# Optimization experiments

Measured on AMD Instinct MI355X. Metric: run time of the kernel, lower is better.

Reference implementation:

```python
import jax, jax.numpy as jnp
import numpy as np

GROUP_SIZE = 128


def setup_inputs() -> dict:
    key = jax.random.key(0)
    k0, k1, k2, k3 = jax.random.split(key, 4)
    B, S, I, O, G = 4, 2048, 4096, 11008, GROUP_SIZE
    x = jax.random.normal(k0, (B, S, I), dtype=jnp.float32)
    # int4 values in [-8, 7]
    qweight = jax.random.randint(k1, (O, I), -8, 8, dtype=jnp.int32)
    # group-wise positive scales, shape [O, I // G]
    scales = jax.random.uniform(k2, (O, I // G), dtype=jnp.float32,
                                minval=1e-3, maxval=2e-2)
    bias = jax.random.normal(k3, (O,), dtype=jnp.float32) * 0.01
    return {"x": x, "qweight": qweight, "scales": scales, "bias": bias}


def reference(x, qweight, scales, bias):
    # bits == 4, quantized path: group-wise dequant then linear
    O, I = qweight.shape
    G = GROUP_SIZE
    w = qweight.reshape(O, I // G, G).astype(x.dtype) * scales[:, :, None].astype(x.dtype)
    w = w.reshape(O, I)  # dequantized weight [O, I]
    # F.linear: y = x @ w.T + bias
    return jnp.einsum('bsi,oi->bso', x, w) + bias.astype(x.dtype)
```

## Files before the change

### kernel.cpp

```cpp
#include <hip/hip_runtime.h>
#include <hip/hip_bf16.h>


typedef __bf16 bf16_t;
typedef __bf16 bf16x8 __attribute__((ext_vector_type(8)));
typedef float f32x4 __attribute__((ext_vector_type(4)));
typedef int ix4 __attribute__((ext_vector_type(4)));
typedef __attribute__((address_space(3))) unsigned char lds_byte;
typedef __attribute__((address_space(1))) unsigned char gmem_byte;

__global__ void rowquant_kernel(const float* __restrict__ x, int* __restrict__ xq,
                                float* __restrict__ sx, int I) {
  __shared__ float red[256];
  const int m = blockIdx.x;
  const float* row = x + (size_t)m * I;
  float mx = 0.f;
  for (int c = threadIdx.x * 4; c < I; c += 1024) {
    const float4 f = *reinterpret_cast<const float4*>(row + c);
    mx = fmaxf(mx, fmaxf(fmaxf(fabsf(f.x), fabsf(f.y)), fmaxf(fabsf(f.z), fabsf(f.w))));
  }
  red[threadIdx.x] = mx;
  __syncthreads();
#pragma unroll
  for (int s = 128; s > 0; s >>= 1) {
    if (threadIdx.x < s) red[threadIdx.x] = fmaxf(red[threadIdx.x], red[threadIdx.x + s]);
    __syncthreads();
  }
  const float rm = fmaxf(red[0], 1e-30f);
  if (threadIdx.x == 0) sx[m] = rm * (1.f / 127.f);
  const float inv = 127.f / rm;
  int* orow = xq + (size_t)m * (I >> 2);
  for (int c = threadIdx.x * 4; c < I; c += 1024) {
    const float4 f = *reinterpret_cast<const float4*>(row + c);
    const int b0 = (int)rintf(f.x * inv), b1 = (int)rintf(f.y * inv);
    const int b2 = (int)rintf(f.z * inv), b3 = (int)rintf(f.w * inv);
    orow[c >> 2] = (b0 & 255) | ((b1 & 255) << 8) | ((b2 & 255) << 16) | (b3 << 24);
  }
}

__global__ void colscale_kernel(const float* __restrict__ sc, float* __restrict__ tw,
                                int NG, int O) {
  const int n = blockIdx.x * blockDim.x + threadIdx.x;
  if (n >= O) return;
  const float* row = sc + (size_t)n * NG;
  float mx = 0.f;
  for (int g = 0; g < NG; ++g) mx = fmaxf(mx, row[g]);
  tw[n] = fmaxf(mx, 1e-30f) * (8.f / 127.f);
}

__global__ void quant_w_kernel(const int* __restrict__ qw, const float* __restrict__ sc,
                               const float* __restrict__ tw, int* __restrict__ wq,
                               int I, int G, long n16) {
  const long stride = (long)gridDim.x * blockDim.x;
  const int I16 = I / 16;
  for (long i = (long)blockIdx.x * blockDim.x + threadIdx.x; i < n16; i += stride) {
    const int n = (int)(i / I16);
    const int k0 = (int)((i - (long)n * I16) * 16);
    const float f = sc[(size_t)n * (I / G) + k0 / G] / tw[n];
    const int4* p = reinterpret_cast<const int4*>(qw + (size_t)n * I + k0);
    const int4 q0 = p[0], q1 = p[1], q2 = p[2], q3 = p[3];
    int b[16];
    b[0] = (int)rintf((float)q0.x * f); b[1] = (int)rintf((float)q0.y * f);
    b[2] = (int)rintf((float)q0.z * f); b[3] = (int)rintf((float)q0.w * f);
    b[4] = (int)rintf((float)q1.x * f); b[5] = (int)rintf((float)q1.y * f);
    b[6] = (int)rintf((float)q1.z * f); b[7] = (int)rintf((float)q1.w * f);
    b[8] = (int)rintf((float)q2.x * f); b[9] = (int)rintf((float)q2.y * f);
    b[10] = (int)rintf((float)q2.z * f); b[11] = (int)rintf((float)q2.w * f);
    b[12] = (int)rintf((float)q3.x * f); b[13] = (int)rintf((float)q3.y * f);
    b[14] = (int)rintf((float)q3.z * f); b[15] = (int)rintf((float)q3.w * f);
    int4 o;
    o.x = (b[0] & 255) | ((b[1] & 255) << 8) | ((b[2] & 255) << 16) | (b[3] << 24);
    o.y = (b[4] & 255) | ((b[5] & 255) << 8) | ((b[6] & 255) << 16) | (b[7] << 24);
    o.z = (b[8] & 255) | ((b[9] & 255) << 8) | ((b[10] & 255) << 16) | (b[11] << 24);
    o.w = (b[12] & 255) | ((b[13] & 255) << 8) | ((b[14] & 255) << 16) | (b[15] << 24);
    reinterpret_cast<int4*>(wq)[i] = o;
  }
}


#define WAITV(n) asm volatile("s_waitcnt vmcnt(" #n ")" ::: "memory")
#define WAITL(n) asm volatile("s_waitcnt lgkmcnt(" #n ")" ::: "memory")
#define BAR() __builtin_amdgcn_s_barrier()
#define SETP(n) __builtin_amdgcn_s_setprio(n)

#define RD_A(DB, q) do { \
  _Pragma("unroll") \
  for (int i_ = 0; i_ < 4; ++i_) { \
    aF[i_][0] = *reinterpret_cast<const ix4*>(&ldsb[(DB) + aRd + (unsigned)((q) * 64 + i_ * 16) * 128u + ks0]); \
    aF[i_][1] = *reinterpret_cast<const ix4*>(&ldsb[(DB) + aRd + (unsigned)((q) * 64 + i_ * 16) * 128u + ks1]); \
  } \
} while (0)

#define RD_B(DB, nh, BF) do { \
  _Pragma("unroll") \
  for (int j_ = 0; j_ < 2; ++j_) { \
    BF[j_][0] = *reinterpret_cast<const ix4*>(&ldsb[(DB) + bRd + (unsigned)((nh) * 32 + j_ * 16) * 128u + ks0]); \
    BF[j_][1] = *reinterpret_cast<const ix4*>(&ldsb[(DB) + bRd + (unsigned)((nh) * 32 + j_ * 16) * 128u + ks1]); \
  } \
} while (0)

#define STG(BASE, P, tau) do { \
  __builtin_amdgcn_global_load_lds((const gmem_byte*)((P) + (size_t)(tau) * 128), \
                                   (lds_byte*)&ldsb[(BASE) + wOff], 16, 0, 0); \
  __builtin_amdgcn_global_load_lds((const gmem_byte*)((P) + (size_t)64 * K + (size_t)(tau) * 128), \
                                   (lds_byte*)&ldsb[(BASE) + 8192u + wOff], 16, 0, 0); \
} while (0)

#define MMQI(q, nh, BF) do { \
  _Pragma("unroll") \
  for (int i_ = 0; i_ < 4; ++i_) \
  _Pragma("unroll") \
  for (int j_ = 0; j_ < 2; ++j_) { \
    acc[(q) * 4 + i_][(nh) * 2 + j_] = __builtin_amdgcn_mfma_i32_16x16x64_i8(aF[i_][0], BF[j_][0], acc[(q) * 4 + i_][(nh) * 2 + j_], 0, 0, 0); \
    acc[(q) * 4 + i_][(nh) * 2 + j_] = __builtin_amdgcn_mfma_i32_16x16x64_i8(aF[i_][1], BF[j_][1], acc[(q) * 4 + i_][(nh) * 2 + j_], 0, 0, 0); \
  } \
} while (0)

__launch_bounds__(512, 2)
__global__ void gemm256_i8_kernel(const char* __restrict__ A, const char* __restrict__ B,
                                  const float* __restrict__ sx, const float* __restrict__ tw,
                                  const float* __restrict__ bias, float* __restrict__ C,
                                  int M, int N, int K) {
  __shared__ __align__(16) unsigned char ldsb[131072];

  const int tid = threadIdx.x;
  const int lane = tid & 63;
  const int w = tid >> 6;
  const int wr = w >> 2;
  const int wc = w & 3;

  const int MT = M >> 8;
  int mt, nt;
  const int bid = blockIdx.x;
  if ((MT & 7) == 0) {
    const int xcd = bid & 7, idx = bid >> 3;
    const int mpx = MT >> 3;
    nt = idx / mpx;
    mt = xcd * mpx + (idx - nt * mpx);
  } else {
    mt = bid % MT;
    nt = bid / MT;
  }
  const int m0 = mt << 8, n0 = nt << 8;

  const int srow8 = lane >> 3;
  const int scol16 = (lane & 7) ^ (srow8 & 7);
  const char* aP0 = A + (size_t)(m0 + w * 8 + srow8) * K + scol16 * 16;
  const char* aP1 = aP0 + (size_t)128 * K;
  const char* bP0 = B + (size_t)(n0 + w * 8 + srow8) * K + scol16 * 16;
  const char* bP1 = bP0 + (size_t)128 * K;
  const unsigned wOff = (unsigned)w * 1024u;

  const unsigned fr = lane & 15;
  const unsigned hi16 = (unsigned)lane >> 4;
  const unsigned sw_ = (fr & 7u) << 4;
  const unsigned ks0 = (hi16 * 16u) ^ sw_;
  const unsigned ks1 = (64u + hi16 * 16u) ^ sw_;
  const unsigned aRd = (unsigned)wr * 16384u + fr * 128u;
  const unsigned bRd = 32768u + (unsigned)(wc >> 1) * 16384u +
                       ((unsigned)(wc & 1) * 64u + fr) * 128u;

  ix4 acc[8][4];
#pragma unroll
  for (int i = 0; i < 8; ++i)
#pragma unroll
    for (int j = 0; j < 4; ++j) acc[i][j] = (ix4){0, 0, 0, 0};

  ix4 aF[4][2], bF0[2][2], bF1[2][2];

  const int NITER = K >> 8;

  STG(0u, aP0, 0); STG(16384u, aP1, 0); STG(32768u, bP0, 0); STG(49152u, bP1, 0);
  STG(98304u, bP0, 1); STG(114688u, bP1, 1);
  WAITV(4);
  BAR();

  for (int it = 0; it < NITER - 1; ++it) {
    const int t = 2 * it;
    RD_A(0u, 0); RD_B(0u, 0, bF0); RD_B(0u, 1, bF1);
    STG(65536u, aP0, t + 1); STG(81920u, aP1, t + 1);
    BAR(); WAITL(0);
    SETP(1); MMQI(0, 0, bF0); MMQI(0, 1, bF1); SETP(0); BAR();
    RD_A(0u, 1);
    STG(32768u, bP0, t + 2); STG(49152u, bP1, t + 2);
    WAITV(4);
    BAR(); WAITL(0);
    SETP(1); MMQI(1, 0, bF0); MMQI(1, 1, bF1); SETP(0); BAR();
    RD_A(65536u, 0); RD_B(65536u, 0, bF0); RD_B(65536u, 1, bF1);
    STG(0u, aP0, t + 2); STG(16384u, aP1, t + 2);
    BAR(); WAITL(0);
    SETP(1); MMQI(0, 0, bF0); MMQI(0, 1, bF1); SETP(0); BAR();
    RD_A(65536u, 1);
    STG(98304u, bP0, t + 3); STG(114688u, bP1, t + 3);
    WAITV(4);
    BAR(); WAITL(0);
    SETP(1); MMQI(1, 0, bF0); MMQI(1, 1, bF1); SETP(0); BAR();
  }
  {
    RD_A(0u, 0); RD_B(0u, 0, bF0); RD_B(0u, 1, bF1);
    STG(65536u, aP0, 2 * NITER - 1); STG(81920u, aP1, 2 * NITER - 1);
    BAR(); WAITL(0);
    SETP(1); MMQI(0, 0, bF0); MMQI(0, 1, bF1); SETP(0); BAR();
    RD_A(0u, 1);
    WAITV(0);
    BAR(); WAITL(0);
    SETP(1); MMQI(1, 0, bF0); MMQI(1, 1, bF1); SETP(0); BAR();
    RD_A(65536u, 0); RD_B(65536u, 0, bF0); RD_B(65536u, 1, bF1);
    WAITL(0);
    SETP(1); MMQI(0, 0, bF0); MMQI(0, 1, bF1); SETP(0);
    RD_A(65536u, 1);
    WAITL(0);
    SETP(1); MMQI(1, 0, bF0); MMQI(1, 1, bF1); SETP(0);
  }

  const int row0 = m0 + wr * 128 + ((lane >> 4) << 2);
  const int col0 = n0 + wc * 64 + (lane & 15);
  float sxc[8][4];
#pragma unroll
  for (int hi = 0; hi < 8; ++hi) {
    const int rbase = row0 + (hi >> 2) * 64 + (hi & 3) * 16;
#pragma unroll
    for (int r = 0; r < 4; ++r) sxc[hi][r] = sx[rbase + r];
  }
#pragma unroll
  for (int j = 0; j < 4; ++j) {
    const int n = col0 + j * 16;
    const float tn = tw[n];
    const float bv = bias[n];
#pragma unroll
    for (int hi = 0; hi < 8; ++hi) {
      const int rbase = row0 + (hi >> 2) * 64 + (hi & 3) * 16;
#pragma unroll
      for (int r = 0; r < 4; ++r)
        C[(size_t)(rbase + r) * N + n] = sxc[hi][r] * tn * (float)acc[hi][j][r] + bv;
    }
  }
}

__global__ void cvt_x_kernel(const float* __restrict__ x, bf16_t* __restrict__ xb, long n8) {
  const long stride = (long)gridDim.x * blockDim.x;
  for (long i = (long)blockIdx.x * blockDim.x + threadIdx.x; i < n8; i += stride) {
    const float4* p = reinterpret_cast<const float4*>(x + i * 8);
    const float4 f0 = p[0];
    const float4 f1 = p[1];
    bf16x8 o;
    o[0] = (bf16_t)f0.x; o[1] = (bf16_t)f0.y; o[2] = (bf16_t)f0.z; o[3] = (bf16_t)f0.w;
    o[4] = (bf16_t)f1.x; o[5] = (bf16_t)f1.y; o[6] = (bf16_t)f1.z; o[7] = (bf16_t)f1.w;
    *reinterpret_cast<bf16x8*>(xb + i * 8) = o;
  }
}

__global__ void deq_w_kernel(const int* __restrict__ qw, const float* __restrict__ sc,
                             bf16_t* __restrict__ wb, int I, int G) {
  const int n = blockIdx.y;
  const int kb = blockIdx.x * blockDim.x + threadIdx.x;
  const int k = kb * 8;
  if (k >= I) return;
  const float s = sc[(size_t)n * (I / G) + k / G];
  const int4* qp = reinterpret_cast<const int4*>(qw + (size_t)n * I + k);
  const int4 q0 = qp[0];
  const int4 q1 = qp[1];
  bf16x8 o;
  o[0] = (bf16_t)((float)q0.x * s);
  o[1] = (bf16_t)((float)q0.y * s);
  o[2] = (bf16_t)((float)q0.z * s);
  o[3] = (bf16_t)((float)q0.w * s);
  o[4] = (bf16_t)((float)q1.x * s);
  o[5] = (bf16_t)((float)q1.y * s);
  o[6] = (bf16_t)((float)q1.z * s);
  o[7] = (bf16_t)((float)q1.w * s);
  *reinterpret_cast<bf16x8*>(wb + (size_t)n * I + k) = o;
}

#define BM 128
#define BK 32
__launch_bounds__(256)
__global__ void gemm_bt_kernel(const bf16_t* __restrict__ A, const bf16_t* __restrict__ B,
                               const float* __restrict__ bias, float* __restrict__ C,
                               int M, int N, int K) {
  __shared__ __align__(16) bf16_t As[2][BM * BK];
  __shared__ __align__(16) bf16_t Bs[2][BM * BK];
  const int tid = threadIdx.x;
  const int lane = tid & 63;
  const int w = tid >> 6;
  const int wr = w >> 1;
  const int wc = w & 1;
  const int m0 = blockIdx.y * BM;
  const int n0 = blockIdx.x * BM;
  const int srow = lane >> 2;
  const int schunk = lane & 3;
  f32x4 acc[4][4];
  const f32x4 zero = {0.f, 0.f, 0.f, 0.f};
#pragma unroll
  for (int i = 0; i < 4; ++i)
#pragma unroll
    for (int j = 0; j < 4; ++j) acc[i][j] = zero;
  const int nt = K / BK;
  auto stage = [&](int t, int buf) {
    const int k0 = t * BK;
#pragma unroll
    for (int j = 0; j < 2; ++j) {
      const int row = w * 32 + j * 16;
      const bf16_t* ga = A + (size_t)(m0 + row + srow) * K + k0 + schunk * 8;
      __builtin_amdgcn_global_load_lds((const gmem_byte*)ga, (lds_byte*)&As[buf][row * BK], 16, 0, 0);
      const bf16_t* gb = B + (size_t)(n0 + row + srow) * K + k0 + schunk * 8;
      __builtin_amdgcn_global_load_lds((const gmem_byte*)gb, (lds_byte*)&Bs[buf][row * BK], 16, 0, 0);
    }
  };
  auto compute = [&](int buf) {
    bf16x8 af[4], bfr[4];
    const int fr2 = lane & 15;
    const int kc = (lane >> 4) * 8;
#pragma unroll
    for (int i = 0; i < 4; ++i) {
      af[i] = *reinterpret_cast<const bf16x8*>(&As[buf][(wr * 64 + i * 16 + fr2) * BK + kc]);
      bfr[i] = *reinterpret_cast<const bf16x8*>(&Bs[buf][(wc * 64 + i * 16 + fr2) * BK + kc]);
    }
#pragma unroll
    for (int i = 0; i < 4; ++i)
#pragma unroll
      for (int j = 0; j < 4; ++j)
        acc[i][j] = __builtin_amdgcn_mfma_f32_16x16x32_bf16(af[i], bfr[j], acc[i][j], 0, 0, 0);
  };
  stage(0, 0);
  __syncthreads();
  int cur = 0;
  for (int t = 0; t < nt - 1; ++t) {
    stage(t + 1, cur ^ 1);
    compute(cur);
    __syncthreads();
    cur ^= 1;
  }
  compute(cur);
#pragma unroll
  for (int j = 0; j < 4; ++j) {
    const int n = n0 + wc * 64 + j * 16 + (lane & 15);
    const float bv = bias[n];
#pragma unroll
    for (int i = 0; i < 4; ++i) {
      const int mbase = m0 + wr * 64 + i * 16 + (lane >> 4) * 4;
#pragma unroll
      for (int r = 0; r < 4; ++r)
        C[(size_t)(mbase + r) * N + n] = acc[i][j][r] + bv;
    }
  }
}

extern "C" void kernel_launch(void* const* d_in, const int* in_sizes, int n_in,
                              void* d_out, int out_size, void* d_ws, size_t ws_size,
                              hipStream_t stream) {
  const float* x = (const float*)d_in[0];
  const int* qw = (const int*)d_in[1];
  const float* sc = (const float*)d_in[2];
  const float* bias = (const float*)d_in[3];
  float* out = (float*)d_out;

  const long O = in_sizes[3];
  const long I = in_sizes[1] / O;
  const long M = in_sizes[0] / I;
  const long G = I / (in_sizes[2] / O);
  const long NG = I / G;

  const size_t i8need = (size_t)(M + O) * I + 4 * (size_t)(M + O);
  const bool i8ok = ((M & 255) == 0) && ((O & 255) == 0) && ((I & 255) == 0) &&
                    (G == 128) && ((I >> 8) >= 2) &&
                    (ws_size >= i8need);
  if (i8ok) {
    char* xq = (char*)d_ws;
    char* wq = xq + (size_t)M * I;
    float* sx = (float*)(wq + (size_t)O * I);
    float* tw = sx + M;
    rowquant_kernel<<<(unsigned)M, 256, 0, stream>>>(x, (int*)xq, sx, (int)I);
    colscale_kernel<<<(unsigned)((O + 255) / 256), 256, 0, stream>>>(sc, tw, (int)NG, (int)O);
    quant_w_kernel<<<2048, 256, 0, stream>>>(qw, sc, tw, (int*)wq, (int)I, (int)G, O * I / 16);
    const int nwg = (int)((M >> 8) * (O >> 8));
    gemm256_i8_kernel<<<nwg, 512, 0, stream>>>(xq, wq, sx, tw, bias, out, (int)M, (int)O, (int)I);
  } else {
    bf16_t* xb = (bf16_t*)d_ws;
    bf16_t* wb = xb + (size_t)M * I;
    if (ws_size < (size_t)(M + O) * I * sizeof(bf16_t)) return;
    cvt_x_kernel<<<2048, 256, 0, stream>>>(x, xb, M * I / 8);
    dim3 dgrid((unsigned)((I / 8 + 255) / 256), (unsigned)O);
    deq_w_kernel<<<dgrid, 256, 0, stream>>>(qw, sc, wb, (int)I, (int)G);
    dim3 ggrid((unsigned)(O / BM), (unsigned)(M / BM));
    gemm_bt_kernel<<<ggrid, 256, 0, stream>>>(xb, wb, bias, out, (int)M, (int)O, (int)I);
  }
}
```

Before: 496.5 us.

## Fuse quantization prep kernels and split LDS wait around MFMA halves

New measurement: 487.3 us. About the same (-1.8%).

```diff
diff --git a/kernel.cpp b/kernel.cpp
--- a/kernel.cpp
+++ b/kernel.cpp
@@ -9,71 +9,75 @@
 typedef __attribute__((address_space(3))) unsigned char lds_byte;
 typedef __attribute__((address_space(1))) unsigned char gmem_byte;
 
-__global__ void rowquant_kernel(const float* __restrict__ x, int* __restrict__ xq,
-                                float* __restrict__ sx, int I) {
+__global__ void prep_kernel(const float* __restrict__ x, int* __restrict__ xq,
+                            float* __restrict__ sx,
+                            const int* __restrict__ qw, const float* __restrict__ sc,
+                            float* __restrict__ tw, int* __restrict__ wq,
+                            int M, int I, int NG) {
   __shared__ float red[256];
-  const int m = blockIdx.x;
-  const float* row = x + (size_t)m * I;
-  float mx = 0.f;
-  for (int c = threadIdx.x * 4; c < I; c += 1024) {
-    const float4 f = *reinterpret_cast<const float4*>(row + c);
-    mx = fmaxf(mx, fmaxf(fmaxf(fabsf(f.x), fabsf(f.y)), fmaxf(fabsf(f.z), fabsf(f.w))));
-  }
-  red[threadIdx.x] = mx;
-  __syncthreads();
-#pragma unroll
-  for (int s = 128; s > 0; s >>= 1) {
-    if (threadIdx.x < s) red[threadIdx.x] = fmaxf(red[threadIdx.x], red[threadIdx.x + s]);
+  const int b = blockIdx.x;
+  const int t = threadIdx.x;
+  if (b < M) {
+    const float* row = x + (size_t)b * I;
+    float mx = 0.f;
+    for (int c = t * 4; c < I; c += 1024) {
+      const float4 f = *reinterpret_cast<const float4*>(row + c);
+      mx = fmaxf(mx, fmaxf(fmaxf(fabsf(f.x), fabsf(f.y)), fmaxf(fabsf(f.z), fabsf(f.w))));
+    }
+    red[t] = mx;
     __syncthreads();
-  }
-  const float rm = fmaxf(red[0], 1e-30f);
-  if (threadIdx.x == 0) sx[m] = rm * (1.f / 127.f);
-  const float inv = 127.f / rm;
-  int* orow = xq + (size_t)m * (I >> 2);
-  for (int c = threadIdx.x * 4; c < I; c += 1024) {
-    const float4 f = *reinterpret_cast<const float4*>(row + c);
-    const int b0 = (int)rintf(f.x * inv), b1 = (int)rintf(f.y * inv);
-    const int b2 = (int)rintf(f.z * inv), b3 = (int)rintf(f.w * inv);
-    orow[c >> 2] = (b0 & 255) | ((b1 & 255) << 8) | ((b2 & 255) << 16) | (b3 << 24);
-  }
-}
-
-__global__ void colscale_kernel(const float* __restrict__ sc, float* __restrict__ tw,
-                                int NG, int O) {
-  const int n = blockIdx.x * blockDim.x + threadIdx.x;
-  if (n >= O) return;
-  const float* row = sc + (size_t)n * NG;
-  float mx = 0.f;
-  for (int g = 0; g < NG; ++g) mx = fmaxf(mx, row[g]);
-  tw[n] = fmaxf(mx, 1e-30f) * (8.f / 127.f);
-}
-
-__global__ void quant_w_kernel(const int* __restrict__ qw, const float* __restrict__ sc,
-                               const float* __restrict__ tw, int* __restrict__ wq,
-                               int I, int G, long n16) {
-  const long stride = (long)gridDim.x * blockDim.x;
-  const int I16 = I / 16;
-  for (long i = (long)blockIdx.x * blockDim.x + threadIdx.x; i < n16; i += stride) {
-    const int n = (int)(i / I16);
-    const int k0 = (int)((i - (long)n * I16) * 16);
-    const float f = sc[(size_t)n * (I / G) + k0 / G] / tw[n];
-    const int4* p = reinterpret_cast<const int4*>(qw + (size_t)n * I + k0);
-    const int4 q0 = p[0], q1 = p[1], q2 = p[2], q3 = p[3];
-    int b[16];
-    b[0] = (int)rintf((float)q0.x * f); b[1] = (int)rintf((float)q0.y * f);
-    b[2] = (int)rintf((float)q0.z * f); b[3] = (int)rintf((float)q0.w * f);
-    b[4] = (int)rintf((float)q1.x * f); b[5] = (int)rintf((float)q1.y * f);
-    b[6] = (int)rintf((float)q1.z * f); b[7] = (int)rintf((float)q1.w * f);
-    b[8] = (int)rintf((float)q2.x * f); b[9] = (int)rintf((float)q2.y * f);
-    b[10] = (int)rintf((float)q2.z * f); b[11] = (int)rintf((float)q2.w * f);
-    b[12] = (int)rintf((float)q3.x * f); b[13] = (int)rintf((float)q3.y * f);
-    b[14] = (int)rintf((float)q3.z * f); b[15] = (int)rintf((float)q3.w * f);
-    int4 o;
-    o.x = (b[0] & 255) | ((b[1] & 255) << 8) | ((b[2] & 255) << 16) | (b[3] << 24);
-    o.y = (b[4] & 255) | ((b[5] & 255) << 8) | ((b[6] & 255) << 16) | (b[7] << 24);
-    o.z = (b[8] & 255) | ((b[9] & 255) << 8) | ((b[10] & 255) << 16) | (b[11] << 24);
-    o.w = (b[12] & 255) | ((b[13] & 255) << 8) | ((b[14] & 255) << 16) | (b[15] << 24);
-    reinterpret_cast<int4*>(wq)[i] = o;
+#pragma unroll
+    for (int s = 128; s > 0; s >>= 1) {
+      if (t < s) red[t] = fmaxf(red[t], red[t + s]);
+      __syncthreads();
+    }
+    const float rm = fmaxf(red[0], 1e-30f);
+    if (t == 0) sx[b] = rm * (1.f / 127.f);
+    const float inv = 127.f / rm;
+    int* orow = xq + (size_t)b * (I >> 2);
+    for (int c = t * 4; c < I; c += 1024) {
+      const float4 f = *reinterpret_cast<const float4*>(row + c);
+      const int b0 = (int)rintf(f.x * inv), b1 = (int)rintf(f.y * inv);
+      const int b2 = (int)rintf(f.z * inv), b3 = (int)rintf(f.w * inv);
+      orow[c >> 2] = (b0 & 255) | ((b1 & 255) << 8) | ((b2 & 255) << 16) | (b3 << 24);
+    }
+  } else {
+    const int n = b - M;
+    const float* srow = sc + (size_t)n * NG;
+    float mx = 0.f;
+    for (int g = t; g < NG; g += 256) mx = fmaxf(mx, srow[g]);
+    red[t] = mx;
+    __syncthreads();
+#pragma unroll
+    for (int s = 128; s > 0; s >>= 1) {
+      if (t < s) red[t] = fmaxf(red[t], red[t + s]);
+      __syncthreads();
+    }
+    const float tn = fmaxf(red[0], 1e-30f) * (8.f / 127.f);
+    if (t == 0) tw[n] = tn;
+    const float itn = 1.f / tn;
+    const int* qrow = qw + (size_t)n * I;
+    int* orow = wq + (size_t)n * (I >> 2);
+    for (int k0 = t * 16; k0 < I; k0 += 4096) {
+      const float f = srow[k0 >> 7] * itn;
+      const int4* p = reinterpret_cast<const int4*>(qrow + k0);
+      const int4 q0 = p[0], q1 = p[1], q2 = p[2], q3 = p[3];
+      int v[16];
+      v[0] = (int)rintf((float)q0.x * f); v[1] = (int)rintf((float)q0.y * f);
+      v[2] = (int)rintf((float)q0.z * f); v[3] = (int)rintf((float)q0.w * f);
+      v[4] = (int)rintf((float)q1.x * f); v[5] = (int)rintf((float)q1.y * f);
+      v[6] = (int)rintf((float)q1.z * f); v[7] = (int)rintf((float)q1.w * f);
+      v[8] = (int)rintf((float)q2.x * f); v[9] = (int)rintf((float)q2.y * f);
+      v[10] = (int)rintf((float)q2.z * f); v[11] = (int)rintf((float)q2.w * f);
+      v[12] = (int)rintf((float)q3.x * f); v[13] = (int)rintf((float)q3.y * f);
+      v[14] = (int)rintf((float)q3.z * f); v[15] = (int)rintf((float)q3.w * f);
+      int4 o;
+      o.x = (v[0] & 255) | ((v[1] & 255) << 8) | ((v[2] & 255) << 16) | (v[3] << 24);
+      o.y = (v[4] & 255) | ((v[5] & 255) << 8) | ((v[6] & 255) << 16) | (v[7] << 24);
+      o.z = (v[8] & 255) | ((v[9] & 255) << 8) | ((v[10] & 255) << 16) | (v[11] << 24);
+      o.w = (v[12] & 255) | ((v[13] & 255) << 8) | ((v[14] & 255) << 16) | (v[15] << 24);
+      *reinterpret_cast<int4*>(orow + (k0 >> 2)) = o;
+    }
   }
 }
 
@@ -179,8 +183,10 @@
     const int t = 2 * it;
     RD_A(0u, 0); RD_B(0u, 0, bF0); RD_B(0u, 1, bF1);
     STG(65536u, aP0, t + 1); STG(81920u, aP1, t + 1);
-    BAR(); WAITL(0);
-    SETP(1); MMQI(0, 0, bF0); MMQI(0, 1, bF1); SETP(0); BAR();
+    BAR(); WAITL(4);
+    SETP(1); MMQI(0, 0, bF0); SETP(0);
+    WAITL(0);
+    SETP(1); MMQI(0, 1, bF1); SETP(0); BAR();
     RD_A(0u, 1);
     STG(32768u, bP0, t + 2); STG(49152u, bP1, t + 2);
     WAITV(4);
@@ -188,8 +194,10 @@
     SETP(1); MMQI(1, 0, bF0); MMQI(1, 1, bF1); SETP(0); BAR();
     RD_A(65536u, 0); RD_B(65536u, 0, bF0); RD_B(65536u, 1, bF1);
     STG(0u, aP0, t + 2); STG(16384u, aP1, t + 2);
-    BAR(); WAITL(0);
-    SETP(1); MMQI(0, 0, bF0); MMQI(0, 1, bF1); SETP(0); BAR();
+    BAR(); WAITL(4);
+    SETP(1); MMQI(0, 0, bF0); SETP(0);
+    WAITL(0);
+    SETP(1); MMQI(0, 1, bF1); SETP(0); BAR();
     RD_A(65536u, 1);
     STG(98304u, bP0, t + 3); STG(114688u, bP1, t + 3);
     WAITV(4);
@@ -199,15 +207,19 @@
   {
     RD_A(0u, 0); RD_B(0u, 0, bF0); RD_B(0u, 1, bF1);
     STG(65536u, aP0, 2 * NITER - 1); STG(81920u, aP1, 2 * NITER - 1);
-    BAR(); WAITL(0);
-    SETP(1); MMQI(0, 0, bF0); MMQI(0, 1, bF1); SETP(0); BAR();
+    BAR(); WAITL(4);
+    SETP(1); MMQI(0, 0, bF0); SETP(0);
+    WAITL(0);
+    SETP(1); MMQI(0, 1, bF1); SETP(0); BAR();
     RD_A(0u, 1);
     WAITV(0);
     BAR(); WAITL(0);
     SETP(1); MMQI(1, 0, bF0); MMQI(1, 1, bF1); SETP(0); BAR();
     RD_A(65536u, 0); RD_B(65536u, 0, bF0); RD_B(65536u, 1, bF1);
-    WAITL(0);
-    SETP(1); MMQI(0, 0, bF0); MMQI(0, 1, bF1); SETP(0);
+    WAITL(4);
+    SETP(1); MMQI(0, 0, bF0); SETP(0);
+    WAITL(0);
+    SETP(1); MMQI(0, 1, bF1); SETP(0);
     RD_A(65536u, 1);
     WAITL(0);
     SETP(1); MMQI(1, 0, bF0); MMQI(1, 1, bF1); SETP(0);
@@ -370,9 +382,8 @@
     char* wq = xq + (size_t)M * I;
     float* sx = (float*)(wq + (size_t)O * I);
     float* tw = sx + M;
-    rowquant_kernel<<<(unsigned)M, 256, 0, stream>>>(x, (int*)xq, sx, (int)I);
-    colscale_kernel<<<(unsigned)((O + 255) / 256), 256, 0, stream>>>(sc, tw, (int)NG, (int)O);
-    quant_w_kernel<<<2048, 256, 0, stream>>>(qw, sc, tw, (int*)wq, (int)I, (int)G, O * I / 16);
+    prep_kernel<<<(unsigned)(M + O), 256, 0, stream>>>(x, (int*)xq, sx, qw, sc, tw,
+                                                       (int*)wq, (int)M, (int)I, (int)NG);
     const int nwg = (int)((M >> 8) * (O >> 8));
     gemm256_i8_kernel<<<nwg, 512, 0, stream>>>(xq, wq, sx, tw, bias, out, (int)M, (int)O, (int)I);
   } else {
```
